# Kernel optimization log

Hardware: AMD Instinct MI355X
Metric: run time of the kernel (lower is better)

## Reference

```python
import jax, jax.numpy as jnp
import numpy as np

B, T, C = 8, 4096, 768


def wkv(w, u, k, v):
    """RWKV WKV linear recurrence with running max/exp state.
    w, u: (C,) ; k, v: (B, T, C) -> y: (B, T, C), all float32.
    Faithful to wkv_pytorch: note w is ADDED to pp (no negation/exp).
    """
    kt = jnp.swapaxes(k, 0, 1)  # (T, B, C)
    vt = jnp.swapaxes(v, 0, 1)

    def step(carry, inp):
        aa, bb, pp = carry            # each (B, C)
        k_t, v_t = inp                # each (B, C)
        ww = u[None, :] + k_t
        p = jnp.maximum(pp, ww)
        e1 = jnp.exp(pp - p)
        e2 = jnp.exp(ww - p)
        y_t = (e1 * aa + e2 * v_t) / (e1 * bb + e2)
        ww2 = w[None, :] + pp
        p2 = jnp.maximum(ww2, k_t)
        e1b = jnp.exp(ww2 - p2)
        e2b = jnp.exp(k_t - p2)
        aa = e1b * aa + e2b * v_t
        bb = e1b * bb + e2b
        return (aa, bb, p2), y_t

    init = (jnp.zeros((B, C), jnp.float32),
            jnp.zeros((B, C), jnp.float32),
            jnp.full((B, C), -1e38, jnp.float32))
    _, y = jax.lax.scan(step, init, (kt, vt))
    return jnp.swapaxes(y, 0, 1)  # (B, T, C)


def setup_inputs() -> dict:
    key = jax.random.key(0)
    ks = jax.random.split(key, 7)
    scale = 1.0 / np.sqrt(C)
    x = jax.random.normal(ks[0], (B, T, C), jnp.float32)
    w_key = jax.random.normal(ks[1], (C, C), jnp.float32) * scale
    w_value = jax.random.normal(ks[2], (C, C), jnp.float32) * scale
    w_receptance = jax.random.normal(ks[3], (C, C), jnp.float32) * scale
    w_output = jax.random.normal(ks[4], (C, C), jnp.float32) * scale
    # 'fancy' init, layer_id=5, n_layer=12
    layer_id, n_layer = 5, 12
    ratio_0_to_1 = layer_id / (n_layer - 1)
    h = np.arange(C, dtype=np.float64)
    spatial_decay = (-5.0 + 8.0 * (h / (C - 1)) ** (0.7 + 1.3 * ratio_0_to_1)).astype(np.float32)
    zigzag = (np.array([(i + 1) % 3 - 1 for i in range(C)], dtype=np.float64) * 0.5)
    spatial_first = (np.ones(C) * np.log(0.3) + zigzag).astype(np.float32)
    return {
        "x": x,
        "w_key": w_key,
        "w_value": w_value,
        "w_receptance": w_receptance,
        "w_output": w_output,
        "spatial_decay": jnp.asarray(spatial_decay),
        "spatial_first": jnp.asarray(spatial_first),
    }


def reference(x, w_key, w_value, w_receptance, w_output, spatial_decay, spatial_first):
    # shift_pixel=0, empty spatial_shift_list -> xk = xv = xr = x
    k = jnp.einsum('btc,oc->bto', x, w_key)
    v = jnp.einsum('btc,oc->bto', x, w_value)
    sr = jax.nn.sigmoid(jnp.einsum('btc,oc->bto', x, w_receptance))
    y = wkv(spatial_decay / T, spatial_first / T, k, v)
    out = jnp.einsum('btc,oc->bto', sr * y, w_output)
    return out
```

## Files before the change

### kernel.cpp

```cpp
#include <hip/hip_runtime.h>
#include <hip/hip_bf16.h>

using bf16 = __hip_bfloat16;
typedef short bf16x8v  __attribute__((ext_vector_type(8)));
typedef float f32x16v  __attribute__((ext_vector_type(16)));

#define GLD_LDS16(g, l) __builtin_amdgcn_global_load_lds(                      \
    (const __attribute__((address_space(1))) void*)(g),                        \
    (__attribute__((address_space(3))) void*)(l), 16, 0, 0)

__device__ __forceinline__ float bflo(unsigned int u) {
  union { unsigned int i; float f; } c; c.i = u << 16; return c.f;
}
__device__ __forceinline__ float bfhi(unsigned int u) {
  union { unsigned int i; float f; } c; c.i = u & 0xffff0000u; return c.f;
}
__device__ __forceinline__ unsigned int packbf(float a, float b) {
  return (unsigned int)(__hip_bfloat16_raw(__float2bfloat16(a)).x) |
         ((unsigned int)(__hip_bfloat16_raw(__float2bfloat16(b)).x) << 16);
}
__device__ __forceinline__ unsigned short bfraw(float a) {
  return __hip_bfloat16_raw(__float2bfloat16(a)).x;
}

__global__ void f2b4_all(const float* __restrict__ x,  const float* __restrict__ wk,
                         const float* __restrict__ wv, const float* __restrict__ wr,
                         const float* __restrict__ wo,
                         bf16* __restrict__ x_bf, bf16* __restrict__ wcat,
                         bf16* __restrict__ wo_bf) {
  int i = blockIdx.x * blockDim.x + threadIdx.x;
  const float* s; bf16* d; int idx;
  if (i < 6291456) { s = x; d = x_bf; idx = i; }
  else {
    int j = i - 6291456;
    int seg = j / 147456;
    idx = j - seg * 147456;
    if (seg == 0)      { s = wk; d = wcat; }
    else if (seg == 1) { s = wv; d = wcat + 589824; }
    else if (seg == 2) { s = wr; d = wcat + 1179648; }
    else               { s = wo; d = wo_bf; }
  }
  const float4 f = reinterpret_cast<const float4*>(s)[idx];
  struct B4 { bf16 a, b, c, d; };
  B4 o = { __float2bfloat16(f.x), __float2bfloat16(f.y),
           __float2bfloat16(f.z), __float2bfloat16(f.w) };
  reinterpret_cast<B4*>(d)[idx] = o;
}

__device__ __forceinline__ void stg64(
    const bf16* __restrict__ A, const bf16* __restrict__ W,
    bf16* la, bf16* lb, int k0, size_t m0, int n0,
    const int srow[4], const int scol[4], int tid)
{
#pragma unroll
  for (int q = 0; q < 4; ++q) {
    GLD_LDS16(A + (m0 + srow[q]) * 768 + k0 + scol[q],
              &la[(size_t)(tid + q * 256) * 8]);
    GLD_LDS16(W + ((size_t)n0 + srow[q]) * 768 + k0 + scol[q],
              &lb[(size_t)(tid + q * 256) * 8]);
  }
}

__device__ __forceinline__ void comp64(
    const bf16* la, const bf16* lb, int wr, int wc, int l31, int hi,
    f32x16v acc[2][2])
{
#pragma unroll
  for (int ks = 0; ks < 4; ++ks) {
    const int gl = ks * 2 + hi;
    bf16x8v av[2], bv[2];
#pragma unroll
    for (int i = 0; i < 2; ++i) {
      const int ra = wr + 32 * i + l31;
      av[i] = *(const bf16x8v*)&la[ra * 64 + ((gl ^ (ra & 7)) * 8)];
    }
#pragma unroll
    for (int j = 0; j < 2; ++j) {
      const int rb = wc + 32 * j + l31;
      bv[j] = *(const bf16x8v*)&lb[rb * 64 + ((gl ^ (rb & 7)) * 8)];
    }
#pragma unroll
    for (int i = 0; i < 2; ++i)
#pragma unroll
      for (int j = 0; j < 2; ++j)
        acc[i][j] = __builtin_amdgcn_mfma_f32_32x32x16_bf16(bv[j], av[i], acc[i][j], 0, 0, 0);
  }
}

__device__ __forceinline__ void gemm_tile_acc(
    const bf16* __restrict__ A, const bf16* __restrict__ W,
    bf16* lds, int tid, size_t m0, int n0, f32x16v acc[2][2])
{
  bf16* const a0 = lds;
  bf16* const b0 = lds + 8192;
  bf16* const a1 = lds + 16384;
  bf16* const b1 = lds + 24576;

  const int lane = tid & 63;
  const int wave = tid >> 6;
  const int l31  = lane & 31;
  const int hi   = lane >> 5;
  const int wr   = (wave >> 1) * 64;
  const int wc   = (wave & 1) * 64;

  int srow[4], scol[4];
#pragma unroll
  for (int q = 0; q < 4; ++q) {
    const int s = tid + q * 256;
    srow[q] = s >> 3;
    scol[q] = (((s & 7) ^ (srow[q] & 7)) * 8);
  }

#pragma unroll
  for (int i = 0; i < 2; ++i)
#pragma unroll
    for (int j = 0; j < 2; ++j)
#pragma unroll
      for (int r = 0; r < 16; ++r) acc[i][j][r] = 0.0f;

  stg64(A, W, a0, b0, 0, m0, n0, srow, scol, tid);

  for (int t = 0; t < 12; t += 2) {
    __syncthreads();
    if (t + 1 < 12) stg64(A, W, a1, b1, (t + 1) * 64, m0, n0, srow, scol, tid);
    comp64(a0, b0, wr, wc, l31, hi, acc);
    __syncthreads();
    if (t + 2 < 12) stg64(A, W, a0, b0, (t + 2) * 64, m0, n0, srow, scol, tid);
    comp64(a1, b1, wr, wc, l31, hi, acc);
  }
}


__global__ __launch_bounds__(256) void gemm_kvr(
    const bf16* __restrict__ A, const bf16* __restrict__ Wcat,
    bf16* __restrict__ Kb, bf16* __restrict__ Vb, bf16* __restrict__ SRb)
{
  __shared__ __align__(16) bf16 lds[32768];
  const int tid = threadIdx.x;
  const int bx = blockIdx.x;
  const int chunk = bx / 1152;
  const int rem   = bx % 1152;
  const int mm    = rem & 63;
  const int nt    = rem >> 6;
  const size_t m0 = (size_t)(chunk * 64 + mm) * 128;
  const int n0 = nt * 128;

  f32x16v acc[2][2];
  gemm_tile_acc(A, Wcat, lds, tid, m0, n0, acc);

  const int seg   = n0 / 768;
  const int ncol0 = n0 - seg * 768;
  bf16* __restrict__ dst = (seg == 0) ? Kb : (seg == 1) ? Vb : SRb;
  const int lane = tid & 63, wave = tid >> 6;
  const int l31 = lane & 31, hi = lane >> 5;
  const int wr = (wave >> 1) * 64, wc = (wave & 1) * 64;

  __syncthreads();
  unsigned short* et = (unsigned short*)lds;
#pragma unroll
  for (int i = 0; i < 2; ++i) {
    const int row_l = wr + 32 * i + l31;
#pragma unroll
    for (int j = 0; j < 2; ++j) {
      const int cb = wc + 32 * j + 4 * hi;
#pragma unroll
      for (int rr = 0; rr < 4; ++rr) {
        float v0 = acc[i][j][4 * rr + 0], v1 = acc[i][j][4 * rr + 1];
        float v2 = acc[i][j][4 * rr + 2], v3 = acc[i][j][4 * rr + 3];
        if (seg == 2) {
          v0 = 1.0f / (1.0f + __expf(-v0)); v1 = 1.0f / (1.0f + __expf(-v1));
          v2 = 1.0f / (1.0f + __expf(-v2)); v3 = 1.0f / (1.0f + __expf(-v3));
        }
        ushort4 pk = { bfraw(v0), bfraw(v1), bfraw(v2), bfraw(v3) };
        *(ushort4*)&et[row_l * 136 + cb + 8 * rr] = pk;
      }
    }
  }
  __syncthreads();
#pragma unroll
  for (int it = 0; it < 8; ++it) {
    const int ci = it * 256 + tid;
    const int r  = ci >> 4;
    const int c8 = (ci & 15) * 8;
    const uint4 w = *(const uint4*)&et[r * 136 + c8];
    *(uint4*)&dst[(m0 + r) * 768 + ncol0 + c8] = w;
  }
}

__global__ __launch_bounds__(256) void gemm_out(
    const bf16* __restrict__ A, const bf16* __restrict__ W,
    float* __restrict__ out)
{
  __shared__ __align__(16) bf16 lds[32768];
  const int tid = threadIdx.x;
  const int bx = blockIdx.x;
  const int chunk = bx / 384;
  const int rem   = bx % 384;
  const int mm    = rem & 63;
  const int nt    = rem >> 6;
  const size_t m0 = (size_t)(chunk * 64 + mm) * 128;
  const int n0 = nt * 128;

  f32x16v acc[2][2];
  gemm_tile_acc(A, W, lds, tid, m0, n0, acc);

  const int lane = tid & 63, wave = tid >> 6;
  const int l31 = lane & 31, hi = lane >> 5;
  const int wr = (wave >> 1) * 64, wc = (wave & 1) * 64;

  __syncthreads();
  float* ef = (float*)lds;
  for (int h = 0; h < 2; ++h) {
    if ((wave >> 1) == h) {
#pragma unroll
      for (int i = 0; i < 2; ++i) {
        const int row_l = 32 * i + l31;
#pragma unroll
        for (int j = 0; j < 2; ++j) {
          const int cb = wc + 32 * j + 4 * hi;
#pragma unroll
          for (int rr = 0; rr < 4; ++rr) {
            float4 pk = { acc[i][j][4 * rr + 0], acc[i][j][4 * rr + 1],
                          acc[i][j][4 * rr + 2], acc[i][j][4 * rr + 3] };
            *(float4*)&ef[row_l * 136 + cb + 8 * rr] = pk;
          }
        }
      }
    }
    __syncthreads();
#pragma unroll
    for (int it = 0; it < 8; ++it) {
      const int ci = it * 256 + tid;
      const int r  = ci >> 5;
      const int c4 = (ci & 31) * 4;
      const float4 w = *(const float4*)&ef[r * 136 + c4];
      *(float4*)&out[(m0 + h * 64 + r) * 768 + n0 + c4] = w;
    }
    __syncthreads();
  }
}

__global__ void wkv_phaseA(const bf16* __restrict__ K, const bf16* __restrict__ V,
                           const float* __restrict__ sd,
                           float* __restrict__ sA, float* __restrict__ sB, float* __restrict__ sP)
{
  const int idx = blockIdx.x * 256 + threadIdx.x;
  const int c4 = idx % 192;
  const int bg = idx / 192;
  const int g  = bg & 127;
  const int b  = bg >> 7;
  const int c0 = c4 * 4;
  float w[4], aa[4], bb[4], pp[4];
#pragma unroll
  for (int e = 0; e < 4; ++e) {
    w[e] = sd[c0 + e] * (1.0f / 4096.0f);
    aa[e] = 0.f; bb[e] = 0.f; pp[e] = -1e38f;
  }
  const size_t base = ((size_t)b * 4096 + (size_t)g * 32) * 768 + c0;
  const uint2* Kp = (const uint2*)(K + base);
  const uint2* Vp = (const uint2*)(V + base);
#pragma unroll 4
  for (int t = 0; t < 32; ++t) {
    const uint2 ku = Kp[(size_t)t * 192];
    const uint2 vu = Vp[(size_t)t * 192];
    const float kc[4] = { bflo(ku.x), bfhi(ku.x), bflo(ku.y), bfhi(ku.y) };
    const float vc[4] = { bflo(vu.x), bfhi(vu.x), bflo(vu.y), bfhi(vu.y) };
#pragma unroll
    for (int e = 0; e < 4; ++e) {
      const float ww2 = w[e] + pp[e];
      const float p2  = fmaxf(ww2, kc[e]);
      const float e1b = __expf(ww2 - p2);
      const float e2b = __expf(kc[e] - p2);
      aa[e] = e1b * aa[e] + e2b * vc[e];
      bb[e] = e1b * bb[e] + e2b;
      pp[e] = p2;
    }
  }
  const int o = g * 6144 + b * 768 + c0;
#pragma unroll
  for (int e = 0; e < 4; ++e) { sA[o + e] = aa[e]; sB[o + e] = bb[e]; sP[o + e] = pp[e]; }
}

__global__ __launch_bounds__(256) void wkv_phaseB(
    const float* __restrict__ sA, const float* __restrict__ sB,
    const float* __restrict__ sP,
    float* __restrict__ iA, float* __restrict__ iB, float* __restrict__ iP,
    const float* __restrict__ sd)
{
  __shared__ float la[128][64], lb[128][64], lp[128][64];
  const int bc0 = blockIdx.x * 64;
  const int tid = threadIdx.x;
  const int gr = tid >> 6;
  const int cc = tid & 63;
  for (int g0 = 0; g0 < 128; g0 += 4) {
    const int g = g0 + gr;
    const int o = g * 6144 + bc0 + cc;
    la[g][cc] = sA[o]; lb[g][cc] = sB[o]; lp[g][cc] = sP[o];
  }
  __syncthreads();
  if (tid < 64) {
    const int c = bc0 + tid;
    const float Lw = 32.0f * (sd[c % 768] * (1.0f / 4096.0f));
    float aa = 0.f, bb = 0.f, pp = -1e38f;
    for (int g = 0; g < 128; ++g) {
      const int o = g * 6144 + c;
      iA[o] = aa; iB[o] = bb; iP[o] = pp;
      const float lag = la[g][tid], lbg = lb[g][tid], lpg = lp[g][tid];
      const float pd = pp + Lw;
      const float pn = fmaxf(pd, lpg);
      const float e0 = __expf(pd - pn);
      const float e1 = __expf(lpg - pn);
      aa = e0 * aa + e1 * lag;
      bb = e0 * bb + e1 * lbg;
      pp = pn;
    }
  }
}

__global__ void wkv_phaseC(const bf16* __restrict__ K, const bf16* __restrict__ V,
                           const bf16* __restrict__ SR,
                           const float* __restrict__ iA, const float* __restrict__ iB,
                           const float* __restrict__ iP,
                           const float* __restrict__ sd, const float* __restrict__ sf,
                           bf16* __restrict__ RY)
{
  const int idx = blockIdx.x * 256 + threadIdx.x;
  const int c4 = idx % 192;
  const int bg = idx / 192;
  const int g  = bg & 127;
  const int b  = bg >> 7;
  const int c0 = c4 * 4;
  const int o = g * 6144 + b * 768 + c0;
  float w[4], u[4], aa[4], bb[4], pp[4];
#pragma unroll
  for (int e = 0; e < 4; ++e) {
    w[e] = sd[c0 + e] * (1.0f / 4096.0f);
    u[e] = sf[c0 + e] * (1.0f / 4096.0f);
    aa[e] = iA[o + e]; bb[e] = iB[o + e]; pp[e] = iP[o + e];
  }
  const size_t base = ((size_t)b * 4096 + (size_t)g * 32) * 768 + c0;
  const uint2* Kp = (const uint2*)(K + base);
  const uint2* Vp = (const uint2*)(V + base);
  const uint2* Sp = (const uint2*)(SR + base);
  uint2* Rp = (uint2*)(RY + base);
#pragma unroll 4
  for (int t = 0; t < 32; ++t) {
    const uint2 ku = Kp[(size_t)t * 192];
    const uint2 vu = Vp[(size_t)t * 192];
    const uint2 su = Sp[(size_t)t * 192];
    const float kc[4] = { bflo(ku.x), bfhi(ku.x), bflo(ku.y), bfhi(ku.y) };
    const float vc[4] = { bflo(vu.x), bfhi(vu.x), bflo(vu.y), bfhi(vu.y) };
    const float sc[4] = { bflo(su.x), bfhi(su.x), bflo(su.y), bfhi(su.y) };
    float y[4];
#pragma unroll
    for (int e = 0; e < 4; ++e) {
      const float ww = u[e] + kc[e];
      const float p  = fmaxf(pp[e], ww);
      const float e1 = __expf(pp[e] - p);
      const float e2 = __expf(ww - p);
      y[e] = (e1 * aa[e] + e2 * vc[e]) / (e1 * bb[e] + e2) * sc[e];
      const float ww2 = w[e] + pp[e];
      const float p2  = fmaxf(ww2, kc[e]);
      const float e1b = __expf(ww2 - p2);
      const float e2b = __expf(kc[e] - p2);
      aa[e] = e1b * aa[e] + e2b * vc[e];
      bb[e] = e1b * bb[e] + e2b;
      pp[e] = p2;
    }
    uint2 r; r.x = packbf(y[0], y[1]); r.y = packbf(y[2], y[3]);
    Rp[(size_t)t * 192] = r;
  }
}

extern "C" void kernel_launch(void* const* d_in, const int* in_sizes, int n_in,
                              void* d_out, int out_size, void* d_ws, size_t ws_size,
                              hipStream_t stream)
{
  const float* x  = (const float*)d_in[0];
  const float* wk = (const float*)d_in[1];
  const float* wv = (const float*)d_in[2];
  const float* wr = (const float*)d_in[3];
  const float* wo = (const float*)d_in[4];
  const float* sd = (const float*)d_in[5];
  const float* sf = (const float*)d_in[6];
  float* out = (float*)d_out;

  char* ws = (char*)d_ws;
  bf16*  x_bf  = (bf16*) (ws + 0);
  bf16*  wcat  = (bf16*) (ws + 50331648);
  bf16*  wo_bf = (bf16*) (ws + 53870592);
  bf16*  Kb    = (bf16*) (ws + 55050240);
  bf16*  Vb    = (bf16*) (ws + 105381888);
  bf16*  SRb   = (bf16*) (ws + 155713536);
  float* sumA  = (float*)(ws + 206045184);
  float* sumB  = (float*)(ws + 209190912);
  float* sumP  = (float*)(ws + 212336640);
  float* iniA  = (float*)(ws + 215482368);
  float* iniB  = (float*)(ws + 218628096);
  float* iniP  = (float*)(ws + 221773824);
  bf16*  ry_bf = x_bf;

  f2b4_all<<<26880, 256, 0, stream>>>(x, wk, wv, wr, wo, x_bf, wcat, wo_bf);

  gemm_kvr<<<4608, 256, 0, stream>>>(x_bf, wcat, Kb, Vb, SRb);

  wkv_phaseA<<<768, 256, 0, stream>>>(Kb, Vb, sd, sumA, sumB, sumP);
  wkv_phaseB<<<96, 256, 0, stream>>>(sumA, sumB, sumP, iniA, iniB, iniP, sd);
  wkv_phaseC<<<768, 256, 0, stream>>>(Kb, Vb, SRb, iniA, iniB, iniP, sd, sf, ry_bf);

  gemm_out<<<1536, 256, 0, stream>>>(ry_bf, wo_bf, out);
}
```

Measured before the change: 440.3 us.

## Load GEMM weight fragments directly from global memory instead of LDS staging

The weight (B) operand of both GEMMs is no longer staged through shared memory; each lane reads its bf16x8 fragment straight from global memory (relying on L2/L1 caching, since weights are reused across many blocks). This halves LDS usage per block (down to 17408 elements, kept for the epilogue), which may allow more blocks per CU. The cost is uncoalesced, latency-exposed global loads inside the MFMA inner loop, with no prefetch overlap for the B operand.

```diff
diff --git a/kernel.cpp b/kernel.cpp
--- a/kernel.cpp
+++ b/kernel.cpp
@@ -47,39 +47,32 @@
   reinterpret_cast<B4*>(d)[idx] = o;
 }
 
-__device__ __forceinline__ void stg64(
-    const bf16* __restrict__ A, const bf16* __restrict__ W,
-    bf16* la, bf16* lb, int k0, size_t m0, int n0,
+__device__ __forceinline__ void stgA(
+    const bf16* __restrict__ A, bf16* la, int k0, size_t m0,
     const int srow[4], const int scol[4], int tid)
 {
 #pragma unroll
-  for (int q = 0; q < 4; ++q) {
+  for (int q = 0; q < 4; ++q)
     GLD_LDS16(A + (m0 + srow[q]) * 768 + k0 + scol[q],
               &la[(size_t)(tid + q * 256) * 8]);
-    GLD_LDS16(W + ((size_t)n0 + srow[q]) * 768 + k0 + scol[q],
-              &lb[(size_t)(tid + q * 256) * 8]);
-  }
 }
 
 __device__ __forceinline__ void comp64(
-    const bf16* la, const bf16* lb, int wr, int wc, int l31, int hi,
-    f32x16v acc[2][2])
+    const bf16* la, const bf16* __restrict__ Wp0, const bf16* __restrict__ Wp1,
+    int k0, int wr, int l31, int hi, f32x16v acc[2][2])
 {
 #pragma unroll
   for (int ks = 0; ks < 4; ++ks) {
     const int gl = ks * 2 + hi;
     bf16x8v av[2], bv[2];
+    bv[0] = *(const bf16x8v*)(Wp0 + k0 + ks * 16);
+    bv[1] = *(const bf16x8v*)(Wp1 + k0 + ks * 16);
 #pragma unroll
     for (int i = 0; i < 2; ++i) {
       const int ra = wr + 32 * i + l31;
       av[i] = *(const bf16x8v*)&la[ra * 64 + ((gl ^ (ra & 7)) * 8)];
     }
 #pragma unroll
-    for (int j = 0; j < 2; ++j) {
-      const int rb = wc + 32 * j + l31;
-      bv[j] = *(const bf16x8v*)&lb[rb * 64 + ((gl ^ (rb & 7)) * 8)];
-    }
-#pragma unroll
     for (int i = 0; i < 2; ++i)
 #pragma unroll
       for (int j = 0; j < 2; ++j)
@@ -92,9 +85,7 @@
     bf16* lds, int tid, size_t m0, int n0, f32x16v acc[2][2])
 {
   bf16* const a0 = lds;
-  bf16* const b0 = lds + 8192;
-  bf16* const a1 = lds + 16384;
-  bf16* const b1 = lds + 24576;
+  bf16* const a1 = lds + 8192;
 
   const int lane = tid & 63;
   const int wave = tid >> 6;
@@ -103,6 +94,9 @@
   const int wr   = (wave >> 1) * 64;
   const int wc   = (wave & 1) * 64;
 
+  const bf16* __restrict__ Wp0 = W + ((size_t)n0 + wc + l31) * 768 + hi * 8;
+  const bf16* __restrict__ Wp1 = W + ((size_t)n0 + wc + 32 + l31) * 768 + hi * 8;
+
   int srow[4], scol[4];
 #pragma unroll
   for (int q = 0; q < 4; ++q) {
@@ -118,15 +112,15 @@
 #pragma unroll
       for (int r = 0; r < 16; ++r) acc[i][j][r] = 0.0f;
 
-  stg64(A, W, a0, b0, 0, m0, n0, srow, scol, tid);
+  stgA(A, a0, 0, m0, srow, scol, tid);
 
   for (int t = 0; t < 12; t += 2) {
     __syncthreads();
-    if (t + 1 < 12) stg64(A, W, a1, b1, (t + 1) * 64, m0, n0, srow, scol, tid);
-    comp64(a0, b0, wr, wc, l31, hi, acc);
+    if (t + 1 < 12) stgA(A, a1, (t + 1) * 64, m0, srow, scol, tid);
+    comp64(a0, Wp0, Wp1, t * 64, wr, l31, hi, acc);
     __syncthreads();
-    if (t + 2 < 12) stg64(A, W, a0, b0, (t + 2) * 64, m0, n0, srow, scol, tid);
-    comp64(a1, b1, wr, wc, l31, hi, acc);
+    if (t + 2 < 12) stgA(A, a0, (t + 2) * 64, m0, srow, scol, tid);
+    comp64(a1, Wp0, Wp1, (t + 1) * 64, wr, l31, hi, acc);
   }
 }
 
@@ -135,7 +129,7 @@
     const bf16* __restrict__ A, const bf16* __restrict__ Wcat,
     bf16* __restrict__ Kb, bf16* __restrict__ Vb, bf16* __restrict__ SRb)
 {
-  __shared__ __align__(16) bf16 lds[32768];
+  __shared__ __align__(16) bf16 lds[17408];
   const int tid = threadIdx.x;
   const int bx = blockIdx.x;
   const int chunk = bx / 1152;
@@ -191,7 +185,7 @@
     const bf16* __restrict__ A, const bf16* __restrict__ W,
     float* __restrict__ out)
 {
-  __shared__ __align__(16) bf16 lds[32768];
+  __shared__ __align__(16) bf16 lds[17408];
   const int tid = threadIdx.x;
   const int bx = blockIdx.x;
   const int chunk = bx / 384;
```

Result: slower. 563.1 us (+27.9%).

## Enlarge GEMM tiles to 256x128 with 32-wide K steps and new swizzle

Applied to the files above, without the earlier changes.

Both GEMMs change from 128x128 output tiles with K-step 64 to 256x128 tiles with K-step 32. Each wave now holds a 4x2 grid of MFMA accumulators, which raises arithmetic intensity per LDS load and halves the block count. The LDS layout packs two rows per 64-element line with a new XOR swizzle, and the epilogues write out in halves or quarters to fit the smaller LDS footprint. The cost is more accumulator registers, which may lower occupancy, and more barriers per K loop.

```diff
diff --git a/kernel.cpp b/kernel.cpp
--- a/kernel.cpp
+++ b/kernel.cpp
@@ -47,40 +47,41 @@
   reinterpret_cast<B4*>(d)[idx] = o;
 }
 
-__device__ __forceinline__ void stg64(
+__device__ __forceinline__ void stg32(
     const bf16* __restrict__ A, const bf16* __restrict__ W,
-    bf16* la, bf16* lb, int k0, size_t m0, int n0,
-    const int srow[4], const int scol[4], int tid)
-{
-#pragma unroll
-  for (int q = 0; q < 4; ++q) {
-    GLD_LDS16(A + (m0 + srow[q]) * 768 + k0 + scol[q],
-              &la[(size_t)(tid + q * 256) * 8]);
-    GLD_LDS16(W + ((size_t)n0 + srow[q]) * 768 + k0 + scol[q],
-              &lb[(size_t)(tid + q * 256) * 8]);
-  }
-}
-
-__device__ __forceinline__ void comp64(
+    bf16* la, bf16* lb, int k0,
+    const size_t aoff[4], const size_t boff[2], int tid)
+{
+#pragma unroll
+  for (int q = 0; q < 4; ++q)
+    GLD_LDS16(A + aoff[q] + k0, &la[(size_t)(tid + q * 256) * 8]);
+#pragma unroll
+  for (int q = 0; q < 2; ++q)
+    GLD_LDS16(W + boff[q] + k0, &lb[(size_t)(tid + q * 256) * 8]);
+}
+
+__device__ __forceinline__ void comp32(
     const bf16* la, const bf16* lb, int wr, int wc, int l31, int hi,
-    f32x16v acc[2][2])
-{
-#pragma unroll
-  for (int ks = 0; ks < 4; ++ks) {
+    f32x16v acc[4][2])
+{
+#pragma unroll
+  for (int ks = 0; ks < 2; ++ks) {
     const int gl = ks * 2 + hi;
-    bf16x8v av[2], bv[2];
-#pragma unroll
-    for (int i = 0; i < 2; ++i) {
+    bf16x8v av[4], bv[2];
+#pragma unroll
+    for (int i = 0; i < 4; ++i) {
       const int ra = wr + 32 * i + l31;
-      av[i] = *(const bf16x8v*)&la[ra * 64 + ((gl ^ (ra & 7)) * 8)];
+      av[i] = *(const bf16x8v*)&la[(ra >> 1) * 64 + (ra & 1) * 32 +
+                                   ((gl ^ ((ra >> 1) & 3)) * 8)];
     }
 #pragma unroll
     for (int j = 0; j < 2; ++j) {
       const int rb = wc + 32 * j + l31;
-      bv[j] = *(const bf16x8v*)&lb[rb * 64 + ((gl ^ (rb & 7)) * 8)];
-    }
-#pragma unroll
-    for (int i = 0; i < 2; ++i)
+      bv[j] = *(const bf16x8v*)&lb[(rb >> 1) * 64 + (rb & 1) * 32 +
+                                   ((gl ^ ((rb >> 1) & 3)) * 8)];
+    }
+#pragma unroll
+    for (int i = 0; i < 4; ++i)
 #pragma unroll
       for (int j = 0; j < 2; ++j)
         acc[i][j] = __builtin_amdgcn_mfma_f32_32x32x16_bf16(bv[j], av[i], acc[i][j], 0, 0, 0);
@@ -89,44 +90,52 @@
 
 __device__ __forceinline__ void gemm_tile_acc(
     const bf16* __restrict__ A, const bf16* __restrict__ W,
-    bf16* lds, int tid, size_t m0, int n0, f32x16v acc[2][2])
+    bf16* lds, int tid, size_t m0, int n0, f32x16v acc[4][2])
 {
   bf16* const a0 = lds;
   bf16* const b0 = lds + 8192;
-  bf16* const a1 = lds + 16384;
-  bf16* const b1 = lds + 24576;
+  bf16* const a1 = lds + 12288;
+  bf16* const b1 = lds + 20480;
 
   const int lane = tid & 63;
   const int wave = tid >> 6;
   const int l31  = lane & 31;
   const int hi   = lane >> 5;
-  const int wr   = (wave >> 1) * 64;
+  const int wr   = (wave >> 1) * 128;
   const int wc   = (wave & 1) * 64;
 
-  int srow[4], scol[4];
+  size_t aoff[4], boff[2];
 #pragma unroll
   for (int q = 0; q < 4; ++q) {
     const int s = tid + q * 256;
-    srow[q] = s >> 3;
-    scol[q] = (((s & 7) ^ (srow[q] & 7)) * 8);
-  }
-
-#pragma unroll
-  for (int i = 0; i < 2; ++i)
+    const int r = 2 * (s >> 3) + ((s >> 2) & 1);
+    const int c = ((s & 3) ^ ((s >> 3) & 3)) * 8;
+    aoff[q] = (m0 + r) * 768 + c;
+  }
+#pragma unroll
+  for (int q = 0; q < 2; ++q) {
+    const int s = tid + q * 256;
+    const int r = 2 * (s >> 3) + ((s >> 2) & 1);
+    const int c = ((s & 3) ^ ((s >> 3) & 3)) * 8;
+    boff[q] = ((size_t)n0 + r) * 768 + c;
+  }
+
+#pragma unroll
+  for (int i = 0; i < 4; ++i)
 #pragma unroll
     for (int j = 0; j < 2; ++j)
 #pragma unroll
       for (int r = 0; r < 16; ++r) acc[i][j][r] = 0.0f;
 
-  stg64(A, W, a0, b0, 0, m0, n0, srow, scol, tid);
-
-  for (int t = 0; t < 12; t += 2) {
-    __syncthreads();
-    if (t + 1 < 12) stg64(A, W, a1, b1, (t + 1) * 64, m0, n0, srow, scol, tid);
-    comp64(a0, b0, wr, wc, l31, hi, acc);
-    __syncthreads();
-    if (t + 2 < 12) stg64(A, W, a0, b0, (t + 2) * 64, m0, n0, srow, scol, tid);
-    comp64(a1, b1, wr, wc, l31, hi, acc);
+  stg32(A, W, a0, b0, 0, aoff, boff, tid);
+
+  for (int t = 0; t < 24; t += 2) {
+    __syncthreads();
+    if (t + 1 < 24) stg32(A, W, a1, b1, (t + 1) * 32, aoff, boff, tid);
+    comp32(a0, b0, wr, wc, l31, hi, acc);
+    __syncthreads();
+    if (t + 2 < 24) stg32(A, W, a0, b0, (t + 2) * 32, aoff, boff, tid);
+    comp32(a1, b1, wr, wc, l31, hi, acc);
   }
 }
 
@@ -135,17 +144,17 @@
     const bf16* __restrict__ A, const bf16* __restrict__ Wcat,
     bf16* __restrict__ Kb, bf16* __restrict__ Vb, bf16* __restrict__ SRb)
 {
-  __shared__ __align__(16) bf16 lds[32768];
+  __shared__ __align__(16) bf16 lds[24576];
   const int tid = threadIdx.x;
   const int bx = blockIdx.x;
-  const int chunk = bx / 1152;
-  const int rem   = bx % 1152;
-  const int mm    = rem & 63;
-  const int nt    = rem >> 6;
-  const size_t m0 = (size_t)(chunk * 64 + mm) * 128;
+  const int chunk = bx / 576;
+  const int rem   = bx % 576;
+  const int nt    = rem >> 5;
+  const int mm    = rem & 31;
+  const size_t m0 = (size_t)(chunk * 32 + mm) * 256;
   const int n0 = nt * 128;
 
-  f32x16v acc[2][2];
+  f32x16v acc[4][2];
   gemm_tile_acc(A, Wcat, lds, tid, m0, n0, acc);
 
   const int seg   = n0 / 768;
@@ -153,37 +162,41 @@
   bf16* __restrict__ dst = (seg == 0) ? Kb : (seg == 1) ? Vb : SRb;
   const int lane = tid & 63, wave = tid >> 6;
   const int l31 = lane & 31, hi = lane >> 5;
-  const int wr = (wave >> 1) * 64, wc = (wave & 1) * 64;
-
-  __syncthreads();
+  const int wc = (wave & 1) * 64;
+
   unsigned short* et = (unsigned short*)lds;
-#pragma unroll
-  for (int i = 0; i < 2; ++i) {
-    const int row_l = wr + 32 * i + l31;
-#pragma unroll
-    for (int j = 0; j < 2; ++j) {
-      const int cb = wc + 32 * j + 4 * hi;
-#pragma unroll
-      for (int rr = 0; rr < 4; ++rr) {
-        float v0 = acc[i][j][4 * rr + 0], v1 = acc[i][j][4 * rr + 1];
-        float v2 = acc[i][j][4 * rr + 2], v3 = acc[i][j][4 * rr + 3];
-        if (seg == 2) {
-          v0 = 1.0f / (1.0f + __expf(-v0)); v1 = 1.0f / (1.0f + __expf(-v1));
-          v2 = 1.0f / (1.0f + __expf(-v2)); v3 = 1.0f / (1.0f + __expf(-v3));
+  for (int h = 0; h < 2; ++h) {
+    __syncthreads();
+    if ((wave >> 1) == h) {
+#pragma unroll
+      for (int i = 0; i < 4; ++i) {
+        const int r_l = 32 * i + l31;
+#pragma unroll
+        for (int j = 0; j < 2; ++j) {
+          const int cb = wc + 32 * j + 4 * hi;
+#pragma unroll
+          for (int rr = 0; rr < 4; ++rr) {
+            float v0 = acc[i][j][4 * rr + 0], v1 = acc[i][j][4 * rr + 1];
+            float v2 = acc[i][j][4 * rr + 2], v3 = acc[i][j][4 * rr + 3];
+            if (seg == 2) {
+              v0 = 1.0f / (1.0f + __expf(-v0)); v1 = 1.0f / (1.0f + __expf(-v1));
+              v2 = 1.0f / (1.0f + __expf(-v2)); v3 = 1.0f / (1.0f + __expf(-v3));
+            }
+            ushort4 pk = { bfraw(v0), bfraw(v1), bfraw(v2), bfraw(v3) };
+            *(ushort4*)&et[r_l * 136 + cb + 8 * rr] = pk;
+          }
         }
-        ushort4 pk = { bfraw(v0), bfraw(v1), bfraw(v2), bfraw(v3) };
-        *(ushort4*)&et[row_l * 136 + cb + 8 * rr] = pk;
       }
     }
-  }
-  __syncthreads();
-#pragma unroll
-  for (int it = 0; it < 8; ++it) {
-    const int ci = it * 256 + tid;
-    const int r  = ci >> 4;
-    const int c8 = (ci & 15) * 8;
-    const uint4 w = *(const uint4*)&et[r * 136 + c8];
-    *(uint4*)&dst[(m0 + r) * 768 + ncol0 + c8] = w;
+    __syncthreads();
+#pragma unroll
+    for (int it = 0; it < 8; ++it) {
+      const int ci = it * 256 + tid;
+      const int r  = ci >> 4;
+      const int c8 = (ci & 15) * 8;
+      const uint4 w = *(const uint4*)&et[r * 136 + c8];
+      *(uint4*)&dst[(m0 + h * 128 + r) * 768 + ncol0 + c8] = w;
+    }
   }
 }
 
@@ -191,30 +204,32 @@
     const bf16* __restrict__ A, const bf16* __restrict__ W,
     float* __restrict__ out)
 {
-  __shared__ __align__(16) bf16 lds[32768];
+  __shared__ __align__(16) bf16 lds[24576];
   const int tid = threadIdx.x;
   const int bx = blockIdx.x;
-  const int chunk = bx / 384;
-  const int rem   = bx % 384;
-  const int mm    = rem & 63;
-  const int nt    = rem >> 6;
-  const size_t m0 = (size_t)(chunk * 64 + mm) * 128;
+  const int chunk = bx / 192;
+  const int rem   = bx % 192;
+  const int nt    = rem >> 5;
+  const int mm    = rem & 31;
+  const size_t m0 = (size_t)(chunk * 32 + mm) * 256;
   const int n0 = nt * 128;
 
-  f32x16v acc[2][2];
+  f32x16v acc[4][2];
   gemm_tile_acc(A, W, lds, tid, m0, n0, acc);
 
   const int lane = tid & 63, wave = tid >> 6;
   const int l31 = lane & 31, hi = lane >> 5;
-  const int wr = (wave >> 1) * 64, wc = (wave & 1) * 64;
-
-  __syncthreads();
+  const int wc = (wave & 1) * 64;
+
   float* ef = (float*)lds;
-  for (int h = 0; h < 2; ++h) {
-    if ((wave >> 1) == h) {
-#pragma unroll
-      for (int i = 0; i < 2; ++i) {
-        const int row_l = 32 * i + l31;
+  for (int p = 0; p < 4; ++p) {
+    __syncthreads();
+    if ((wave >> 1) == (p >> 1)) {
+      const int i0 = 2 * (p & 1);
+#pragma unroll
+      for (int ii = 0; ii < 2; ++ii) {
+        const int i = i0 + ii;
+        const int r_l = 32 * ii + l31;
 #pragma unroll
         for (int j = 0; j < 2; ++j) {
           const int cb = wc + 32 * j + 4 * hi;
@@ -222,7 +237,7 @@
           for (int rr = 0; rr < 4; ++rr) {
             float4 pk = { acc[i][j][4 * rr + 0], acc[i][j][4 * rr + 1],
                           acc[i][j][4 * rr + 2], acc[i][j][4 * rr + 3] };
-            *(float4*)&ef[row_l * 136 + cb + 8 * rr] = pk;
+            *(float4*)&ef[r_l * 136 + cb + 8 * rr] = pk;
           }
         }
       }
@@ -234,9 +249,8 @@
       const int r  = ci >> 5;
       const int c4 = (ci & 31) * 4;
       const float4 w = *(const float4*)&ef[r * 136 + c4];
-      *(float4*)&out[(m0 + h * 64 + r) * 768 + n0 + c4] = w;
-    }
-    __syncthreads();
+      *(float4*)&out[(m0 + p * 64 + r) * 768 + n0 + c4] = w;
+    }
   }
 }
 
@@ -402,11 +416,11 @@
 
   f2b4_all<<<26880, 256, 0, stream>>>(x, wk, wv, wr, wo, x_bf, wcat, wo_bf);
 
-  gemm_kvr<<<4608, 256, 0, stream>>>(x_bf, wcat, Kb, Vb, SRb);
+  gemm_kvr<<<2304, 256, 0, stream>>>(x_bf, wcat, Kb, Vb, SRb);
 
   wkv_phaseA<<<768, 256, 0, stream>>>(Kb, Vb, sd, sumA, sumB, sumP);
   wkv_phaseB<<<96, 256, 0, stream>>>(sumA, sumB, sumP, iniA, iniB, iniP, sd);
   wkv_phaseC<<<768, 256, 0, stream>>>(Kb, Vb, SRb, iniA, iniB, iniP, sd, sf, ry_bf);
 
-  gemm_out<<<1536, 256, 0, stream>>>(ry_bf, wo_bf, out);
-}
+  gemm_out<<<768, 256, 0, stream>>>(ry_bf, wo_bf, out);
+}
```

Result: slower. 503.0 us (+14.2%).

## Retile KVR GEMM to 256x128 tiles with 512 threads and K=32 stages

Applied to the files above, without the earlier changes.

The fused K/V/R projection GEMM now uses 512-thread blocks computing 256x128 output tiles, with a K step of 32 and a new LDS swizzle that packs two rows per 64-element line. LDS drops to 48KB so more blocks can be resident (launch bounds 512,4), and each B tile is reused across twice as many rows. The epilogue writes the tile in two halves through the smaller LDS buffer. The output GEMM keeps the old pipeline through duplicated helpers. Risks: twice as many barriers per K, and fewer MFMAs per sync.

```diff
diff --git a/kernel.cpp b/kernel.cpp
--- a/kernel.cpp
+++ b/kernel.cpp
@@ -47,37 +47,36 @@
   reinterpret_cast<B4*>(d)[idx] = o;
 }
 
-__device__ __forceinline__ void stg64(
+__device__ __forceinline__ void stg32k(
     const bf16* __restrict__ A, const bf16* __restrict__ W,
-    bf16* la, bf16* lb, int k0, size_t m0, int n0,
-    const int srow[4], const int scol[4], int tid)
-{
-#pragma unroll
-  for (int q = 0; q < 4; ++q) {
-    GLD_LDS16(A + (m0 + srow[q]) * 768 + k0 + scol[q],
-              &la[(size_t)(tid + q * 256) * 8]);
-    GLD_LDS16(W + ((size_t)n0 + srow[q]) * 768 + k0 + scol[q],
-              &lb[(size_t)(tid + q * 256) * 8]);
-  }
-}
-
-__device__ __forceinline__ void comp64(
+    bf16* la, bf16* lb, int k0,
+    const size_t aoff[2], size_t boff, int tid)
+{
+#pragma unroll
+  for (int q = 0; q < 2; ++q)
+    GLD_LDS16(A + aoff[q] + k0, &la[(size_t)(tid + q * 512) * 8]);
+  GLD_LDS16(W + boff + k0, &lb[(size_t)tid * 8]);
+}
+
+__device__ __forceinline__ void comp32k(
     const bf16* la, const bf16* lb, int wr, int wc, int l31, int hi,
     f32x16v acc[2][2])
 {
 #pragma unroll
-  for (int ks = 0; ks < 4; ++ks) {
+  for (int ks = 0; ks < 2; ++ks) {
     const int gl = ks * 2 + hi;
     bf16x8v av[2], bv[2];
 #pragma unroll
     for (int i = 0; i < 2; ++i) {
       const int ra = wr + 32 * i + l31;
-      av[i] = *(const bf16x8v*)&la[ra * 64 + ((gl ^ (ra & 7)) * 8)];
+      av[i] = *(const bf16x8v*)&la[(ra >> 1) * 64 + (ra & 1) * 32 +
+                                   ((gl ^ ((ra >> 1) & 3)) * 8)];
     }
 #pragma unroll
     for (int j = 0; j < 2; ++j) {
       const int rb = wc + 32 * j + l31;
-      bv[j] = *(const bf16x8v*)&lb[rb * 64 + ((gl ^ (rb & 7)) * 8)];
+      bv[j] = *(const bf16x8v*)&lb[(rb >> 1) * 64 + (rb & 1) * 32 +
+                                   ((gl ^ ((rb >> 1) & 3)) * 8)];
     }
 #pragma unroll
     for (int i = 0; i < 2; ++i)
@@ -87,14 +86,24 @@
   }
 }
 
-__device__ __forceinline__ void gemm_tile_acc(
-    const bf16* __restrict__ A, const bf16* __restrict__ W,
-    bf16* lds, int tid, size_t m0, int n0, f32x16v acc[2][2])
-{
+__global__ __launch_bounds__(512, 4) void gemm_kvr(
+    const bf16* __restrict__ A, const bf16* __restrict__ Wcat,
+    bf16* __restrict__ Kb, bf16* __restrict__ Vb, bf16* __restrict__ SRb)
+{
+  __shared__ __align__(16) bf16 lds[24576];
+  const int tid = threadIdx.x;
+  const int bx = blockIdx.x;
+  const int chunk = bx / 576;
+  const int rem   = bx % 576;
+  const int nt    = rem >> 5;
+  const int mm    = rem & 31;
+  const size_t m0 = (size_t)(chunk * 32 + mm) * 256;
+  const int n0 = nt * 128;
+
   bf16* const a0 = lds;
   bf16* const b0 = lds + 8192;
-  bf16* const a1 = lds + 16384;
-  bf16* const b1 = lds + 24576;
+  bf16* const a1 = lds + 12288;
+  bf16* const b1 = lds + 20480;
 
   const int lane = tid & 63;
   const int wave = tid >> 6;
@@ -103,14 +112,22 @@
   const int wr   = (wave >> 1) * 64;
   const int wc   = (wave & 1) * 64;
 
-  int srow[4], scol[4];
-#pragma unroll
-  for (int q = 0; q < 4; ++q) {
-    const int s = tid + q * 256;
-    srow[q] = s >> 3;
-    scol[q] = (((s & 7) ^ (srow[q] & 7)) * 8);
-  }
-
+  size_t aoff[2], boff;
+#pragma unroll
+  for (int q = 0; q < 2; ++q) {
+    const int s = tid + q * 512;
+    const int r = 2 * (s >> 3) + ((s >> 2) & 1);
+    const int c = ((s & 3) ^ ((s >> 3) & 3)) * 8;
+    aoff[q] = (m0 + r) * 768 + c;
+  }
+  {
+    const int s = tid;
+    const int r = 2 * (s >> 3) + ((s >> 2) & 1);
+    const int c = ((s & 3) ^ ((s >> 3) & 3)) * 8;
+    boff = ((size_t)n0 + r) * 768 + c;
+  }
+
+  f32x16v acc[2][2];
 #pragma unroll
   for (int i = 0; i < 2; ++i)
 #pragma unroll
@@ -118,72 +135,95 @@
 #pragma unroll
       for (int r = 0; r < 16; ++r) acc[i][j][r] = 0.0f;
 
-  stg64(A, W, a0, b0, 0, m0, n0, srow, scol, tid);
-
-  for (int t = 0; t < 12; t += 2) {
-    __syncthreads();
-    if (t + 1 < 12) stg64(A, W, a1, b1, (t + 1) * 64, m0, n0, srow, scol, tid);
-    comp64(a0, b0, wr, wc, l31, hi, acc);
-    __syncthreads();
-    if (t + 2 < 12) stg64(A, W, a0, b0, (t + 2) * 64, m0, n0, srow, scol, tid);
-    comp64(a1, b1, wr, wc, l31, hi, acc);
-  }
-}
-
-
-__global__ __launch_bounds__(256) void gemm_kvr(
-    const bf16* __restrict__ A, const bf16* __restrict__ Wcat,
-    bf16* __restrict__ Kb, bf16* __restrict__ Vb, bf16* __restrict__ SRb)
-{
-  __shared__ __align__(16) bf16 lds[32768];
-  const int tid = threadIdx.x;
-  const int bx = blockIdx.x;
-  const int chunk = bx / 1152;
-  const int rem   = bx % 1152;
-  const int mm    = rem & 63;
-  const int nt    = rem >> 6;
-  const size_t m0 = (size_t)(chunk * 64 + mm) * 128;
-  const int n0 = nt * 128;
-
-  f32x16v acc[2][2];
-  gemm_tile_acc(A, Wcat, lds, tid, m0, n0, acc);
+  stg32k(A, Wcat, a0, b0, 0, aoff, boff, tid);
+
+  for (int t = 0; t < 24; t += 2) {
+    __syncthreads();
+    if (t + 1 < 24) stg32k(A, Wcat, a1, b1, (t + 1) * 32, aoff, boff, tid);
+    comp32k(a0, b0, wr, wc, l31, hi, acc);
+    __syncthreads();
+    if (t + 2 < 24) stg32k(A, Wcat, a0, b0, (t + 2) * 32, aoff, boff, tid);
+    comp32k(a1, b1, wr, wc, l31, hi, acc);
+  }
 
   const int seg   = n0 / 768;
   const int ncol0 = n0 - seg * 768;
   bf16* __restrict__ dst = (seg == 0) ? Kb : (seg == 1) ? Vb : SRb;
-  const int lane = tid & 63, wave = tid >> 6;
-  const int l31 = lane & 31, hi = lane >> 5;
-  const int wr = (wave >> 1) * 64, wc = (wave & 1) * 64;
-
-  __syncthreads();
+
   unsigned short* et = (unsigned short*)lds;
-#pragma unroll
-  for (int i = 0; i < 2; ++i) {
-    const int row_l = wr + 32 * i + l31;
+  for (int h = 0; h < 2; ++h) {
+    __syncthreads();
+    if ((wave >> 2) == h) {
+      const int r_base = ((wave >> 1) & 1) * 64;
+#pragma unroll
+      for (int i = 0; i < 2; ++i) {
+        const int r_l = r_base + 32 * i + l31;
+#pragma unroll
+        for (int j = 0; j < 2; ++j) {
+          const int cb = wc + 32 * j + 4 * hi;
+#pragma unroll
+          for (int rr = 0; rr < 4; ++rr) {
+            float v0 = acc[i][j][4 * rr + 0], v1 = acc[i][j][4 * rr + 1];
+            float v2 = acc[i][j][4 * rr + 2], v3 = acc[i][j][4 * rr + 3];
+            if (seg == 2) {
+              v0 = 1.0f / (1.0f + __expf(-v0)); v1 = 1.0f / (1.0f + __expf(-v1));
+              v2 = 1.0f / (1.0f + __expf(-v2)); v3 = 1.0f / (1.0f + __expf(-v3));
+            }
+            ushort4 pk = { bfraw(v0), bfraw(v1), bfraw(v2), bfraw(v3) };
+            *(ushort4*)&et[r_l * 136 + cb + 8 * rr] = pk;
+          }
+        }
+      }
+    }
+    __syncthreads();
+#pragma unroll
+    for (int it = 0; it < 4; ++it) {
+      const int ci = it * 512 + tid;
+      const int r  = ci >> 4;
+      const int c8 = (ci & 15) * 8;
+      const uint4 w = *(const uint4*)&et[r * 136 + c8];
+      *(uint4*)&dst[(m0 + h * 128 + r) * 768 + ncol0 + c8] = w;
+    }
+  }
+}
+
+__device__ __forceinline__ void stg64o(
+    const bf16* __restrict__ A, const bf16* __restrict__ W,
+    bf16* la, bf16* lb, int k0, size_t m0, int n0,
+    const int srow[4], const int scol[4], int tid)
+{
+#pragma unroll
+  for (int q = 0; q < 4; ++q) {
+    GLD_LDS16(A + (m0 + srow[q]) * 768 + k0 + scol[q],
+              &la[(size_t)(tid + q * 256) * 8]);
+    GLD_LDS16(W + ((size_t)n0 + srow[q]) * 768 + k0 + scol[q],
+              &lb[(size_t)(tid + q * 256) * 8]);
+  }
+}
+
+__device__ __forceinline__ void comp64o(
+    const bf16* la, const bf16* lb, int wr, int wc, int l31, int hi,
+    f32x16v acc[2][2])
+{
+#pragma unroll
+  for (int ks = 0; ks < 4; ++ks) {
+    const int gl = ks * 2 + hi;
+    bf16x8v av[2], bv[2];
+#pragma unroll
+    for (int i = 0; i < 2; ++i) {
+      const int ra = wr + 32 * i + l31;
+      av[i] = *(const bf16x8v*)&la[ra * 64 + ((gl ^ (ra & 7)) * 8)];
+    }
 #pragma unroll
     for (int j = 0; j < 2; ++j) {
-      const int cb = wc + 32 * j + 4 * hi;
-#pragma unroll
-      for (int rr = 0; rr < 4; ++rr) {
-        float v0 = acc[i][j][4 * rr + 0], v1 = acc[i][j][4 * rr + 1];
-        float v2 = acc[i][j][4 * rr + 2], v3 = acc[i][j][4 * rr + 3];
-        if (seg == 2) {
-          v0 = 1.0f / (1.0f + __expf(-v0)); v1 = 1.0f / (1.0f + __expf(-v1));
-          v2 = 1.0f / (1.0f + __expf(-v2)); v3 = 1.0f / (1.0f + __expf(-v3));
-        }
-        ushort4 pk = { bfraw(v0), bfraw(v1), bfraw(v2), bfraw(v3) };
-        *(ushort4*)&et[row_l * 136 + cb + 8 * rr] = pk;
-      }
-    }
-  }
-  __syncthreads();
-#pragma unroll
-  for (int it = 0; it < 8; ++it) {
-    const int ci = it * 256 + tid;
-    const int r  = ci >> 4;
-    const int c8 = (ci & 15) * 8;
-    const uint4 w = *(const uint4*)&et[r * 136 + c8];
-    *(uint4*)&dst[(m0 + r) * 768 + ncol0 + c8] = w;
+      const int rb = wc + 32 * j + l31;
+      bv[j] = *(const bf16x8v*)&lb[rb * 64 + ((gl ^ (rb & 7)) * 8)];
+    }
+#pragma unroll
+    for (int i = 0; i < 2; ++i)
+#pragma unroll
+      for (int j = 0; j < 2; ++j)
+        acc[i][j] = __builtin_amdgcn_mfma_f32_32x32x16_bf16(bv[j], av[i], acc[i][j], 0, 0, 0);
   }
 }
 
@@ -201,12 +241,43 @@
   const size_t m0 = (size_t)(chunk * 64 + mm) * 128;
   const int n0 = nt * 128;
 
+  bf16* const a0 = lds;
+  bf16* const b0 = lds + 8192;
+  bf16* const a1 = lds + 16384;
+  bf16* const b1 = lds + 24576;
+
+  const int lane = tid & 63;
+  const int wave = tid >> 6;
+  const int l31  = lane & 31;
+  const int hi   = lane >> 5;
+  const int wr   = (wave >> 1) * 64;
+  const int wc   = (wave & 1) * 64;
+
+  int srow[4], scol[4];
+#pragma unroll
+  for (int q = 0; q < 4; ++q) {
+    const int s = tid + q * 256;
+    srow[q] = s >> 3;
+    scol[q] = (((s & 7) ^ (srow[q] & 7)) * 8);
+  }
+
   f32x16v acc[2][2];
-  gemm_tile_acc(A, W, lds, tid, m0, n0, acc);
-
-  const int lane = tid & 63, wave = tid >> 6;
-  const int l31 = lane & 31, hi = lane >> 5;
-  const int wr = (wave >> 1) * 64, wc = (wave & 1) * 64;
+#pragma unroll
+  for (int i = 0; i < 2; ++i)
+#pragma unroll
+    for (int j = 0; j < 2; ++j)
+#pragma unroll
+      for (int r = 0; r < 16; ++r) acc[i][j][r] = 0.0f;
+
+  stg64o(A, W, a0, b0, 0, m0, n0, srow, scol, tid);
+  for (int t = 0; t < 12; t += 2) {
+    __syncthreads();
+    if (t + 1 < 12) stg64o(A, W, a1, b1, (t + 1) * 64, m0, n0, srow, scol, tid);
+    comp64o(a0, b0, wr, wc, l31, hi, acc);
+    __syncthreads();
+    if (t + 2 < 12) stg64o(A, W, a0, b0, (t + 2) * 64, m0, n0, srow, scol, tid);
+    comp64o(a1, b1, wr, wc, l31, hi, acc);
+  }
 
   __syncthreads();
   float* ef = (float*)lds;
@@ -402,7 +473,7 @@
 
   f2b4_all<<<26880, 256, 0, stream>>>(x, wk, wv, wr, wo, x_bf, wcat, wo_bf);
 
-  gemm_kvr<<<4608, 256, 0, stream>>>(x_bf, wcat, Kb, Vb, SRb);
+  gemm_kvr<<<2304, 512, 0, stream>>>(x_bf, wcat, Kb, Vb, SRb);
 
   wkv_phaseA<<<768, 256, 0, stream>>>(Kb, Vb, sd, sumA, sumB, sumP);
   wkv_phaseB<<<96, 256, 0, stream>>>(sumA, sumB, sumP, iniA, iniB, iniP, sd);
```

Result: slower. 453.6 us (+3.0%).
